# Performance work log

Measured on AMD Instinct MI355X. Metric: run time of the kernel, lower is better.

The kernel has to match this reference:

```python
import jax, jax.numpy as jnp
import numpy as np


def setup_inputs() -> dict:
    key = jax.random.key(0)
    k1, k2, k3, k4 = jax.random.split(key, 4)
    B, L, R, H, D = 64, 512, 512, 512, 256
    return {
        "lstm_lt": jax.random.normal(k1, (B, L, H), dtype=jnp.float32),
        "lstm_rt": jax.random.normal(k2, (B, R, H), dtype=jnp.float32),
        "atten_W": jax.random.normal(k3, (H, D), dtype=jnp.float32) * 0.05,
        "diagnoal_W": jax.random.normal(k4, (1, 1, D), dtype=jnp.float32) * 0.05,
    }


def reference(lstm_lt, lstm_rt, atten_W, diagnoal_W):
    # Projection (the original's broadcast-multiply-sum is exactly a GEMM):
    # atten_lt[b,l,d] = tanh(sum_h lstm_lt[b,l,h] * W[h,d]) * diag_W[d]
    atten_lt = jnp.tanh(jnp.einsum('blh,hd->bld', lstm_lt, atten_W)) * diagnoal_W
    atten_rt = jnp.tanh(jnp.einsum('brh,hd->brd', lstm_rt, atten_W))
    # batch_dot over the attention dim -> (B, L, R)
    atten_value = jnp.einsum('bld,brd->blr', atten_lt, atten_rt)
    # No masks supplied (len(inputs)==2 path); softmax over last axis.
    return jax.nn.softmax(atten_value, axis=-1)
```

## Files before the change

kernel.cpp:

```cpp
#include <hip/hip_runtime.h>

typedef __attribute__((ext_vector_type(8))) __bf16 bf16x8;
typedef __attribute__((ext_vector_type(4))) float f32x4;

#define DI __device__ __forceinline__

DI unsigned short f2bf(float x) {
  unsigned u = __float_as_uint(x);
  u += 0x7fffu + ((u >> 16) & 1u);
  return (unsigned short)(u >> 16);
}

DI float tanh_fast(float x) {
  float ax = fabsf(x);
  float e = __expf(-2.0f * ax);
  float t = (1.0f - e) / (1.0f + e);
  return x < 0.0f ? -t : t;
}

__global__ void k_wt(const float* __restrict__ W, unsigned short* __restrict__ Wt) {
  int n = blockIdx.x;
  int t = threadIdx.x;
  int k = t * 4;
  ushort4 v;
  v.x = f2bf(W[(k + 0) * 256 + n]);
  v.y = f2bf(W[(k + 1) * 256 + n]);
  v.z = f2bf(W[(k + 2) * 256 + n]);
  v.w = f2bf(W[(k + 3) * 256 + n]);
  *(ushort4*)&Wt[n * 512 + k] = v;
}

#define G1_LDA 72

__global__ __launch_bounds__(512) void k_proj(
    const float* __restrict__ Alt, const float* __restrict__ Art,
    const unsigned short* __restrict__ Wt, const float* __restrict__ diag,
    unsigned short* __restrict__ Olt, unsigned short* __restrict__ Ort) {
  __shared__ __align__(16) unsigned short As[128 * G1_LDA];
  __shared__ __align__(16) unsigned short Bs[256 * G1_LDA];

  int bx = blockIdx.x;
  bool is_lt = bx < 256;
  int m0 = (is_lt ? bx : bx - 256) * 128;
  const float* A = (is_lt ? Alt : Art) + (size_t)m0 * 512;
  unsigned short* O = (is_lt ? Olt : Ort) + (size_t)m0 * 256;

  int tid  = threadIdx.x;
  int lane = tid & 63;
  int wid  = tid >> 6;
  int wm   = wid >> 2;
  int wn   = wid & 3;
  int l15  = lane & 15;
  int quad = lane >> 4;

  f32x4 zero = {0.0f, 0.0f, 0.0f, 0.0f};
  f32x4 acc[4][4];
#pragma unroll
  for (int i = 0; i < 4; i++)
#pragma unroll
    for (int j = 0; j < 4; j++) acc[i][j] = zero;

  for (int k0 = 0; k0 < 512; k0 += 64) {
#pragma unroll
    for (int i = 0; i < 4; i++) {
      int seg = tid + i * 512;
      int r = seg >> 4;
      int c4 = seg & 15;
      f32x4 f = *(const f32x4*)&A[(size_t)r * 512 + k0 + c4 * 4];
      ushort4 v;
      v.x = f2bf(f.x); v.y = f2bf(f.y); v.z = f2bf(f.z); v.w = f2bf(f.w);
      *(ushort4*)&As[r * G1_LDA + c4 * 4] = v;
    }
#pragma unroll
    for (int i = 0; i < 4; i++) {
      int seg = tid + i * 512;
      int n = seg >> 3;
      int kc = seg & 7;
      *(uint4*)&Bs[n * G1_LDA + kc * 8] = *(const uint4*)&Wt[n * 512 + k0 + kc * 8];
    }
    __syncthreads();

#pragma unroll
    for (int ks = 0; ks < 2; ks++) {
      bf16x8 a[4], b[4];
#pragma unroll
      for (int mt = 0; mt < 4; mt++)
        a[mt] = *(const bf16x8*)&As[(wm * 64 + mt * 16 + l15) * G1_LDA + ks * 32 + quad * 8];
#pragma unroll
      for (int nt = 0; nt < 4; nt++)
        b[nt] = *(const bf16x8*)&Bs[(wn * 64 + nt * 16 + l15) * G1_LDA + ks * 32 + quad * 8];
#pragma unroll
      for (int mt = 0; mt < 4; mt++)
#pragma unroll
        for (int nt = 0; nt < 4; nt++)
          acc[mt][nt] = __builtin_amdgcn_mfma_f32_16x16x32_bf16(a[mt], b[nt], acc[mt][nt], 0, 0, 0);
    }
    __syncthreads();
  }

  float dscale[4];
#pragma unroll
  for (int nt = 0; nt < 4; nt++)
    dscale[nt] = is_lt ? diag[wn * 64 + nt * 16 + l15] : 1.0f;

#pragma unroll
  for (int mt = 0; mt < 4; mt++) {
#pragma unroll
    for (int r = 0; r < 4; r++) {
      int row = wm * 64 + mt * 16 + quad * 4 + r;
#pragma unroll
      for (int nt = 0; nt < 4; nt++) {
        int col = wn * 64 + nt * 16 + l15;
        float t = tanh_fast(acc[mt][nt][r]) * dscale[nt];
        O[(size_t)row * 256 + col] = f2bf(t);
      }
    }
  }
}

#define G2_LD 40

__global__ __launch_bounds__(512) void k_attn(
    const unsigned short* __restrict__ Lt, const unsigned short* __restrict__ Rt,
    float* __restrict__ Out) {
  __shared__ __align__(16) unsigned short Ls[64 * G2_LD];
  __shared__ __align__(16) unsigned short Rs[512 * G2_LD];
  __shared__ float red[8][64];
  __shared__ float rowv[64];

  int bx = blockIdx.x;
  int b  = bx >> 3;
  int l0 = (bx & 7) * 64;
  const unsigned short* Lb = Lt + ((size_t)b * 512 + l0) * 256;
  const unsigned short* Rb = Rt + (size_t)b * 512 * 256;
  float* Ob = Out + ((size_t)b * 512 + l0) * 512;

  int tid  = threadIdx.x;
  int lane = tid & 63;
  int wid  = tid >> 6;
  int l15  = lane & 15;
  int quad = lane >> 4;

  f32x4 zero = {0.0f, 0.0f, 0.0f, 0.0f};
  f32x4 acc[4][4];
#pragma unroll
  for (int i = 0; i < 4; i++)
#pragma unroll
    for (int j = 0; j < 4; j++) acc[i][j] = zero;

  for (int k0 = 0; k0 < 256; k0 += 32) {
    if (tid < 256) {
      int r = tid >> 2, kc = tid & 3;
      *(uint4*)&Ls[r * G2_LD + kc * 8] = *(const uint4*)&Lb[r * 256 + k0 + kc * 8];
    }
#pragma unroll
    for (int i = 0; i < 4; i++) {
      int seg = tid + i * 512;
      int r = seg >> 2, kc = seg & 3;
      *(uint4*)&Rs[r * G2_LD + kc * 8] = *(const uint4*)&Rb[r * 256 + k0 + kc * 8];
    }
    __syncthreads();

    bf16x8 a[4], bb[4];
#pragma unroll
    for (int mt = 0; mt < 4; mt++)
      a[mt] = *(const bf16x8*)&Ls[(mt * 16 + l15) * G2_LD + quad * 8];
#pragma unroll
    for (int nt = 0; nt < 4; nt++)
      bb[nt] = *(const bf16x8*)&Rs[(wid * 64 + nt * 16 + l15) * G2_LD + quad * 8];
#pragma unroll
    for (int mt = 0; mt < 4; mt++)
#pragma unroll
      for (int nt = 0; nt < 4; nt++)
        acc[mt][nt] = __builtin_amdgcn_mfma_f32_16x16x32_bf16(a[mt], bb[nt], acc[mt][nt], 0, 0, 0);
    __syncthreads();
  }

#pragma unroll
  for (int mt = 0; mt < 4; mt++) {
#pragma unroll
    for (int r = 0; r < 4; r++) {
      float m = fmaxf(fmaxf(acc[mt][0][r], acc[mt][1][r]),
                      fmaxf(acc[mt][2][r], acc[mt][3][r]));
      m = fmaxf(m, __shfl_xor(m, 1));
      m = fmaxf(m, __shfl_xor(m, 2));
      m = fmaxf(m, __shfl_xor(m, 4));
      m = fmaxf(m, __shfl_xor(m, 8));
      if (l15 == 0) red[wid][mt * 16 + quad * 4 + r] = m;
    }
  }
  __syncthreads();
  if (tid < 64) {
    float m = red[0][tid];
#pragma unroll
    for (int w = 1; w < 8; w++) m = fmaxf(m, red[w][tid]);
    rowv[tid] = m;
  }
  __syncthreads();

#pragma unroll
  for (int mt = 0; mt < 4; mt++) {
#pragma unroll
    for (int r = 0; r < 4; r++) {
      float base = rowv[mt * 16 + quad * 4 + r];
      float s = 0.0f;
#pragma unroll
      for (int nt = 0; nt < 4; nt++) {
        float e = __expf(acc[mt][nt][r] - base);
        acc[mt][nt][r] = e;
        s += e;
      }
      s += __shfl_xor(s, 1);
      s += __shfl_xor(s, 2);
      s += __shfl_xor(s, 4);
      s += __shfl_xor(s, 8);
      if (l15 == 0) red[wid][mt * 16 + quad * 4 + r] = s;
    }
  }
  __syncthreads();
  if (tid < 64) {
    float s = red[0][tid];
#pragma unroll
    for (int w = 1; w < 8; w++) s += red[w][tid];
    rowv[tid] = 1.0f / s;
  }
  __syncthreads();

#pragma unroll
  for (int mt = 0; mt < 4; mt++) {
#pragma unroll
    for (int r = 0; r < 4; r++) {
      int row = mt * 16 + quad * 4 + r;
      float inv = rowv[row];
#pragma unroll
      for (int nt = 0; nt < 4; nt++) {
        int col = wid * 64 + nt * 16 + l15;
        Ob[(size_t)row * 512 + col] = acc[mt][nt][r] * inv;
      }
    }
  }
}

extern "C" void kernel_launch(void* const* d_in, const int* in_sizes, int n_in,
                              void* d_out, int out_size, void* d_ws, size_t ws_size,
                              hipStream_t stream) {
  const float* lstm_lt = (const float*)d_in[0];
  const float* lstm_rt = (const float*)d_in[1];
  const float* W       = (const float*)d_in[2];
  const float* diag    = (const float*)d_in[3];
  float* out = (float*)d_out;

  unsigned short* Wt  = (unsigned short*)d_ws;
  unsigned short* Olt = (unsigned short*)((char*)d_ws + (size_t)256 * 512 * 2);
  unsigned short* Ort = Olt + (size_t)32768 * 256;

  k_wt<<<dim3(256), dim3(128), 0, stream>>>(W, Wt);
  k_proj<<<dim3(512), dim3(512), 0, stream>>>(lstm_lt, lstm_rt, Wt, diag, Olt, Ort);
  k_attn<<<dim3(512), dim3(512), 0, stream>>>(Olt, Ort, out);
}
```

Baseline: 238.5 us.

## Load MFMA fragments directly from global, drop LDS staging, remap blocks per XCD

Both GEMM kernels stop staging tiles through shared memory. Each wave now loads its bf16 (or fp32-converted) fragments straight from global memory into registers, which removes the per-k-step __syncthreads barriers. Blocks grow to 1024 threads with 32x64 tiles per wave, using launch_bounds(1024, 4). The attention kernel remaps block indices so that all row-blocks of one batch land on the same XCD, which should improve L2 reuse of the right-hand operand. The trade-off is redundant global/L2 reads and less coalesced fp32 loads for the projection input.

```diff
diff --git a/kernel.cpp b/kernel.cpp
--- a/kernel.cpp
+++ b/kernel.cpp
@@ -9,6 +9,13 @@
   unsigned u = __float_as_uint(x);
   u += 0x7fffu + ((u >> 16) & 1u);
   return (unsigned short)(u >> 16);
+}
+
+DI bf16x8 cvt8(f32x4 lo, f32x4 hi) {
+  bf16x8 r;
+  r[0] = (__bf16)lo.x; r[1] = (__bf16)lo.y; r[2] = (__bf16)lo.z; r[3] = (__bf16)lo.w;
+  r[4] = (__bf16)hi.x; r[5] = (__bf16)hi.y; r[6] = (__bf16)hi.z; r[7] = (__bf16)hi.w;
+  return r;
 }
 
 DI float tanh_fast(float x) {
@@ -30,15 +37,10 @@
   *(ushort4*)&Wt[n * 512 + k] = v;
 }
 
-#define G1_LDA 72
-
-__global__ __launch_bounds__(512) void k_proj(
+__global__ __launch_bounds__(1024, 4) void k_proj(
     const float* __restrict__ Alt, const float* __restrict__ Art,
     const unsigned short* __restrict__ Wt, const float* __restrict__ diag,
     unsigned short* __restrict__ Olt, unsigned short* __restrict__ Ort) {
-  __shared__ __align__(16) unsigned short As[128 * G1_LDA];
-  __shared__ __align__(16) unsigned short Bs[256 * G1_LDA];
-
   int bx = blockIdx.x;
   bool is_lt = bx < 256;
   int m0 = (is_lt ? bx : bx - 256) * 128;
@@ -48,89 +50,74 @@
   int tid  = threadIdx.x;
   int lane = tid & 63;
   int wid  = tid >> 6;
-  int wm   = wid >> 2;
-  int wn   = wid & 3;
+  int wmg  = wid >> 2;
+  int wng  = wid & 3;
   int l15  = lane & 15;
   int quad = lane >> 4;
 
+  const float* a0 = A + (size_t)(wmg * 32 + 0 * 16 + l15) * 512 + quad * 8;
+  const float* a1 = A + (size_t)(wmg * 32 + 1 * 16 + l15) * 512 + quad * 8;
+  const unsigned short* bp[4];
+#pragma unroll
+  for (int nt = 0; nt < 4; nt++)
+    bp[nt] = Wt + (size_t)(wng * 64 + nt * 16 + l15) * 512 + quad * 8;
+
   f32x4 zero = {0.0f, 0.0f, 0.0f, 0.0f};
-  f32x4 acc[4][4];
-#pragma unroll
-  for (int i = 0; i < 4; i++)
+  f32x4 acc[2][4];
+#pragma unroll
+  for (int i = 0; i < 2; i++)
 #pragma unroll
     for (int j = 0; j < 4; j++) acc[i][j] = zero;
 
-  for (int k0 = 0; k0 < 512; k0 += 64) {
-#pragma unroll
-    for (int i = 0; i < 4; i++) {
-      int seg = tid + i * 512;
-      int r = seg >> 4;
-      int c4 = seg & 15;
-      f32x4 f = *(const f32x4*)&A[(size_t)r * 512 + k0 + c4 * 4];
-      ushort4 v;
-      v.x = f2bf(f.x); v.y = f2bf(f.y); v.z = f2bf(f.z); v.w = f2bf(f.w);
-      *(ushort4*)&As[r * G1_LDA + c4 * 4] = v;
-    }
-#pragma unroll
-    for (int i = 0; i < 4; i++) {
-      int seg = tid + i * 512;
-      int n = seg >> 3;
-      int kc = seg & 7;
-      *(uint4*)&Bs[n * G1_LDA + kc * 8] = *(const uint4*)&Wt[n * 512 + k0 + kc * 8];
-    }
-    __syncthreads();
-
-#pragma unroll
-    for (int ks = 0; ks < 2; ks++) {
-      bf16x8 a[4], b[4];
-#pragma unroll
-      for (int mt = 0; mt < 4; mt++)
-        a[mt] = *(const bf16x8*)&As[(wm * 64 + mt * 16 + l15) * G1_LDA + ks * 32 + quad * 8];
+#pragma unroll 2
+  for (int k0 = 0; k0 < 512; k0 += 32) {
+    bf16x8 a[2], bb[4];
+    {
+      f32x4 lo0 = *(const f32x4*)(a0 + k0);
+      f32x4 hi0 = *(const f32x4*)(a0 + k0 + 4);
+      f32x4 lo1 = *(const f32x4*)(a1 + k0);
+      f32x4 hi1 = *(const f32x4*)(a1 + k0 + 4);
+      a[0] = cvt8(lo0, hi0);
+      a[1] = cvt8(lo1, hi1);
+    }
+#pragma unroll
+    for (int nt = 0; nt < 4; nt++)
+      bb[nt] = *(const bf16x8*)(bp[nt] + k0);
+#pragma unroll
+    for (int mt = 0; mt < 2; mt++)
 #pragma unroll
       for (int nt = 0; nt < 4; nt++)
-        b[nt] = *(const bf16x8*)&Bs[(wn * 64 + nt * 16 + l15) * G1_LDA + ks * 32 + quad * 8];
-#pragma unroll
-      for (int mt = 0; mt < 4; mt++)
-#pragma unroll
-        for (int nt = 0; nt < 4; nt++)
-          acc[mt][nt] = __builtin_amdgcn_mfma_f32_16x16x32_bf16(a[mt], b[nt], acc[mt][nt], 0, 0, 0);
-    }
-    __syncthreads();
+        acc[mt][nt] = __builtin_amdgcn_mfma_f32_16x16x32_bf16(a[mt], bb[nt], acc[mt][nt], 0, 0, 0);
   }
 
   float dscale[4];
 #pragma unroll
   for (int nt = 0; nt < 4; nt++)
-    dscale[nt] = is_lt ? diag[wn * 64 + nt * 16 + l15] : 1.0f;
-
-#pragma unroll
-  for (int mt = 0; mt < 4; mt++) {
-#pragma unroll
-    for (int r = 0; r < 4; r++) {
-      int row = wm * 64 + mt * 16 + quad * 4 + r;
+    dscale[nt] = is_lt ? diag[wng * 64 + nt * 16 + l15] : 1.0f;
+
+#pragma unroll
+  for (int mt = 0; mt < 2; mt++) {
+#pragma unroll
+    for (int r = 0; r < 4; r++) {
+      int row = wmg * 32 + mt * 16 + quad * 4 + r;
 #pragma unroll
       for (int nt = 0; nt < 4; nt++) {
-        int col = wn * 64 + nt * 16 + l15;
-        float t = tanh_fast(acc[mt][nt][r]) * dscale[nt];
-        O[(size_t)row * 256 + col] = f2bf(t);
+        int col = wng * 64 + nt * 16 + l15;
+        O[(size_t)row * 256 + col] = f2bf(tanh_fast(acc[mt][nt][r]) * dscale[nt]);
       }
     }
   }
 }
 
-#define G2_LD 40
-
-__global__ __launch_bounds__(512) void k_attn(
+__global__ __launch_bounds__(1024, 4) void k_attn(
     const unsigned short* __restrict__ Lt, const unsigned short* __restrict__ Rt,
     float* __restrict__ Out) {
-  __shared__ __align__(16) unsigned short Ls[64 * G2_LD];
-  __shared__ __align__(16) unsigned short Rs[512 * G2_LD];
   __shared__ float red[8][64];
   __shared__ float rowv[64];
 
   int bx = blockIdx.x;
-  int b  = bx >> 3;
-  int l0 = (bx & 7) * 64;
+  int b  = (bx & 7) * 8 + ((bx >> 3) & 7);
+  int l0 = (bx >> 6) * 64;
   const unsigned short* Lb = Lt + ((size_t)b * 512 + l0) * 256;
   const unsigned short* Rb = Rt + (size_t)b * 512 * 256;
   float* Ob = Out + ((size_t)b * 512 + l0) * 512;
@@ -138,46 +125,42 @@
   int tid  = threadIdx.x;
   int lane = tid & 63;
   int wid  = tid >> 6;
+  int wmg  = wid >> 3;
+  int wng  = wid & 7;
   int l15  = lane & 15;
   int quad = lane >> 4;
 
+  const unsigned short* ap0 = Lb + (size_t)(wmg * 32 + 0 * 16 + l15) * 256 + quad * 8;
+  const unsigned short* ap1 = Lb + (size_t)(wmg * 32 + 1 * 16 + l15) * 256 + quad * 8;
+  const unsigned short* bp[4];
+#pragma unroll
+  for (int nt = 0; nt < 4; nt++)
+    bp[nt] = Rb + (size_t)(wng * 64 + nt * 16 + l15) * 256 + quad * 8;
+
   f32x4 zero = {0.0f, 0.0f, 0.0f, 0.0f};
-  f32x4 acc[4][4];
-#pragma unroll
-  for (int i = 0; i < 4; i++)
+  f32x4 acc[2][4];
+#pragma unroll
+  for (int i = 0; i < 2; i++)
 #pragma unroll
     for (int j = 0; j < 4; j++) acc[i][j] = zero;
 
+#pragma unroll 2
   for (int k0 = 0; k0 < 256; k0 += 32) {
-    if (tid < 256) {
-      int r = tid >> 2, kc = tid & 3;
-      *(uint4*)&Ls[r * G2_LD + kc * 8] = *(const uint4*)&Lb[r * 256 + k0 + kc * 8];
-    }
-#pragma unroll
-    for (int i = 0; i < 4; i++) {
-      int seg = tid + i * 512;
-      int r = seg >> 2, kc = seg & 3;
-      *(uint4*)&Rs[r * G2_LD + kc * 8] = *(const uint4*)&Rb[r * 256 + k0 + kc * 8];
-    }
-    __syncthreads();
-
-    bf16x8 a[4], bb[4];
-#pragma unroll
-    for (int mt = 0; mt < 4; mt++)
-      a[mt] = *(const bf16x8*)&Ls[(mt * 16 + l15) * G2_LD + quad * 8];
+    bf16x8 a[2], bb[4];
+    a[0] = *(const bf16x8*)(ap0 + k0);
+    a[1] = *(const bf16x8*)(ap1 + k0);
 #pragma unroll
     for (int nt = 0; nt < 4; nt++)
-      bb[nt] = *(const bf16x8*)&Rs[(wid * 64 + nt * 16 + l15) * G2_LD + quad * 8];
-#pragma unroll
-    for (int mt = 0; mt < 4; mt++)
+      bb[nt] = *(const bf16x8*)(bp[nt] + k0);
+#pragma unroll
+    for (int mt = 0; mt < 2; mt++)
 #pragma unroll
       for (int nt = 0; nt < 4; nt++)
         acc[mt][nt] = __builtin_amdgcn_mfma_f32_16x16x32_bf16(a[mt], bb[nt], acc[mt][nt], 0, 0, 0);
-    __syncthreads();
-  }
-
-#pragma unroll
-  for (int mt = 0; mt < 4; mt++) {
+  }
+
+#pragma unroll
+  for (int mt = 0; mt < 2; mt++) {
 #pragma unroll
     for (int r = 0; r < 4; r++) {
       float m = fmaxf(fmaxf(acc[mt][0][r], acc[mt][1][r]),
@@ -186,7 +169,7 @@
       m = fmaxf(m, __shfl_xor(m, 2));
       m = fmaxf(m, __shfl_xor(m, 4));
       m = fmaxf(m, __shfl_xor(m, 8));
-      if (l15 == 0) red[wid][mt * 16 + quad * 4 + r] = m;
+      if (l15 == 0) red[wng][wmg * 32 + mt * 16 + quad * 4 + r] = m;
     }
   }
   __syncthreads();
@@ -199,10 +182,10 @@
   __syncthreads();
 
 #pragma unroll
-  for (int mt = 0; mt < 4; mt++) {
-#pragma unroll
-    for (int r = 0; r < 4; r++) {
-      float base = rowv[mt * 16 + quad * 4 + r];
+  for (int mt = 0; mt < 2; mt++) {
+#pragma unroll
+    for (int r = 0; r < 4; r++) {
+      float base = rowv[wmg * 32 + mt * 16 + quad * 4 + r];
       float s = 0.0f;
 #pragma unroll
       for (int nt = 0; nt < 4; nt++) {
@@ -214,7 +197,7 @@
       s += __shfl_xor(s, 2);
       s += __shfl_xor(s, 4);
       s += __shfl_xor(s, 8);
-      if (l15 == 0) red[wid][mt * 16 + quad * 4 + r] = s;
+      if (l15 == 0) red[wng][wmg * 32 + mt * 16 + quad * 4 + r] = s;
     }
   }
   __syncthreads();
@@ -227,14 +210,14 @@
   __syncthreads();
 
 #pragma unroll
-  for (int mt = 0; mt < 4; mt++) {
-#pragma unroll
-    for (int r = 0; r < 4; r++) {
-      int row = mt * 16 + quad * 4 + r;
+  for (int mt = 0; mt < 2; mt++) {
+#pragma unroll
+    for (int r = 0; r < 4; r++) {
+      int row = wmg * 32 + mt * 16 + quad * 4 + r;
       float inv = rowv[row];
 #pragma unroll
       for (int nt = 0; nt < 4; nt++) {
-        int col = wid * 64 + nt * 16 + l15;
+        int col = wng * 64 + nt * 16 + l15;
         Ob[(size_t)row * 512 + col] = acc[mt][nt][r] * inv;
       }
     }
@@ -255,6 +238,6 @@
   unsigned short* Ort = Olt + (size_t)32768 * 256;
 
   k_wt<<<dim3(256), dim3(128), 0, stream>>>(W, Wt);
-  k_proj<<<dim3(512), dim3(512), 0, stream>>>(lstm_lt, lstm_rt, Wt, diag, Olt, Ort);
-  k_attn<<<dim3(512), dim3(512), 0, stream>>>(Olt, Ort, out);
-}
+  k_proj<<<dim3(512), dim3(1024), 0, stream>>>(lstm_lt, lstm_rt, Wt, diag, Olt, Ort);
+  k_attn<<<dim3(512), dim3(1024), 0, stream>>>(Olt, Ort, out);
+}
```

After: 311.2 us. +30.5%, slower.

## Load GEMM tiles with direct global-to-LDS transfers and XOR-swizzled layouts

Applied to the files above, without the earlier changes.

Both the projection and attention kernels now fill shared memory with global_load_lds 16-byte direct transfers instead of going through registers. The layout uses XOR swizzles in place of padded strides. The projection kernel now keeps A tiles as fp32 in LDS and converts to bf16 when fragments are read, so register staging and conversion no longer sit on the load path. The attention kernel doubles its K step to 64 and remaps block indices so blocks sharing a batch are spread differently. Launch bounds now ask for higher occupancy, which adds register pressure, and the larger fp32 LDS tile may limit residency.

```diff
diff --git a/kernel.cpp b/kernel.cpp
--- a/kernel.cpp
+++ b/kernel.cpp
@@ -9,6 +9,13 @@
   unsigned u = __float_as_uint(x);
   u += 0x7fffu + ((u >> 16) & 1u);
   return (unsigned short)(u >> 16);
+}
+
+DI bf16x8 cvt8(f32x4 lo, f32x4 hi) {
+  bf16x8 r;
+  r[0] = (__bf16)lo.x; r[1] = (__bf16)lo.y; r[2] = (__bf16)lo.z; r[3] = (__bf16)lo.w;
+  r[4] = (__bf16)hi.x; r[5] = (__bf16)hi.y; r[6] = (__bf16)hi.z; r[7] = (__bf16)hi.w;
+  return r;
 }
 
 DI float tanh_fast(float x) {
@@ -16,6 +23,12 @@
   float e = __expf(-2.0f * ax);
   float t = (1.0f - e) / (1.0f + e);
   return x < 0.0f ? -t : t;
+}
+
+DI void glds16(const void* gptr, void* lptr) {
+  __builtin_amdgcn_global_load_lds(
+      (const __attribute__((address_space(1))) unsigned int*)gptr,
+      (__attribute__((address_space(3))) unsigned int*)lptr, 16, 0, 0);
 }
 
 __global__ void k_wt(const float* __restrict__ W, unsigned short* __restrict__ Wt) {
@@ -30,19 +43,17 @@
   *(ushort4*)&Wt[n * 512 + k] = v;
 }
 
-#define G1_LDA 72
-
-__global__ __launch_bounds__(512) void k_proj(
+__global__ __launch_bounds__(512, 4) void k_proj(
     const float* __restrict__ Alt, const float* __restrict__ Art,
     const unsigned short* __restrict__ Wt, const float* __restrict__ diag,
     unsigned short* __restrict__ Olt, unsigned short* __restrict__ Ort) {
-  __shared__ __align__(16) unsigned short As[128 * G1_LDA];
-  __shared__ __align__(16) unsigned short Bs[256 * G1_LDA];
+  __shared__ __align__(16) float As[128 * 64];
+  __shared__ __align__(16) unsigned short Bs[256 * 64];
 
   int bx = blockIdx.x;
   bool is_lt = bx < 256;
   int m0 = (is_lt ? bx : bx - 256) * 128;
-  const float* A = (is_lt ? Alt : Art) + (size_t)m0 * 512;
+  const char* Abase = (const char*)((is_lt ? Alt : Art) + (size_t)m0 * 512);
   unsigned short* O = (is_lt ? Olt : Ort) + (size_t)m0 * 256;
 
   int tid  = threadIdx.x;
@@ -52,6 +63,16 @@
   int wn   = wid & 3;
   int l15  = lane & 15;
   int quad = lane >> 4;
+  int r7   = l15 & 7;
+
+  int lr4 = lane >> 4, c16 = lane & 15;
+  int aoff = lr4 * 2048 + ((c16 ^ lr4) << 4);
+  int lr8 = lane >> 3, s8 = lane & 7;
+  int boff = lr8 * 1024 + ((s8 ^ lr8) << 4);
+
+  const char* Bbase = (const char*)Wt;
+  char* AsB = (char*)As;
+  char* BsB = (char*)Bs;
 
   f32x4 zero = {0.0f, 0.0f, 0.0f, 0.0f};
   f32x4 acc[4][4];
@@ -63,20 +84,14 @@
   for (int k0 = 0; k0 < 512; k0 += 64) {
 #pragma unroll
     for (int i = 0; i < 4; i++) {
-      int seg = tid + i * 512;
-      int r = seg >> 4;
-      int c4 = seg & 15;
-      f32x4 f = *(const f32x4*)&A[(size_t)r * 512 + k0 + c4 * 4];
-      ushort4 v;
-      v.x = f2bf(f.x); v.y = f2bf(f.y); v.z = f2bf(f.z); v.w = f2bf(f.w);
-      *(ushort4*)&As[r * G1_LDA + c4 * 4] = v;
+      int j = wid * 4 + i;
+      glds16(Abase + (size_t)j * 8192 + (size_t)k0 * 4 + (aoff ^ ((j & 1) << 6)),
+             AsB + j * 1024);
     }
 #pragma unroll
     for (int i = 0; i < 4; i++) {
-      int seg = tid + i * 512;
-      int n = seg >> 3;
-      int kc = seg & 7;
-      *(uint4*)&Bs[n * G1_LDA + kc * 8] = *(const uint4*)&Wt[n * 512 + k0 + kc * 8];
+      int j = wid * 4 + i;
+      glds16(Bbase + (size_t)j * 8192 + (size_t)k0 * 2 + boff, BsB + j * 1024);
     }
     __syncthreads();
 
@@ -84,11 +99,19 @@
     for (int ks = 0; ks < 2; ks++) {
       bf16x8 a[4], b[4];
 #pragma unroll
-      for (int mt = 0; mt < 4; mt++)
-        a[mt] = *(const bf16x8*)&As[(wm * 64 + mt * 16 + l15) * G1_LDA + ks * 32 + quad * 8];
-#pragma unroll
-      for (int nt = 0; nt < 4; nt++)
-        b[nt] = *(const bf16x8*)&Bs[(wn * 64 + nt * 16 + l15) * G1_LDA + ks * 32 + quad * 8];
+      for (int mt = 0; mt < 4; mt++) {
+        int row = wm * 64 + mt * 16 + l15;
+        int c0 = ks * 8 + quad * 2;
+        f32x4 lo = *(const f32x4*)(AsB + row * 256 + (((c0    ) ^ r7) << 4));
+        f32x4 hi = *(const f32x4*)(AsB + row * 256 + (((c0 + 1) ^ r7) << 4));
+        a[mt] = cvt8(lo, hi);
+      }
+#pragma unroll
+      for (int nt = 0; nt < 4; nt++) {
+        int row = wn * 64 + nt * 16 + l15;
+        int c = ks * 4 + quad;
+        b[nt] = *(const bf16x8*)(BsB + row * 128 + ((c ^ r7) << 4));
+      }
 #pragma unroll
       for (int mt = 0; mt < 4; mt++)
 #pragma unroll
@@ -111,28 +134,25 @@
 #pragma unroll
       for (int nt = 0; nt < 4; nt++) {
         int col = wn * 64 + nt * 16 + l15;
-        float t = tanh_fast(acc[mt][nt][r]) * dscale[nt];
-        O[(size_t)row * 256 + col] = f2bf(t);
-      }
-    }
-  }
-}
-
-#define G2_LD 40
-
-__global__ __launch_bounds__(512) void k_attn(
+        O[(size_t)row * 256 + col] = f2bf(tanh_fast(acc[mt][nt][r]) * dscale[nt]);
+      }
+    }
+  }
+}
+
+__global__ __launch_bounds__(512, 4) void k_attn(
     const unsigned short* __restrict__ Lt, const unsigned short* __restrict__ Rt,
     float* __restrict__ Out) {
-  __shared__ __align__(16) unsigned short Ls[64 * G2_LD];
-  __shared__ __align__(16) unsigned short Rs[512 * G2_LD];
+  __shared__ __align__(16) unsigned short Ls[64 * 64];
+  __shared__ __align__(16) unsigned short Rs[512 * 64];
   __shared__ float red[8][64];
   __shared__ float rowv[64];
 
   int bx = blockIdx.x;
-  int b  = bx >> 3;
-  int l0 = (bx & 7) * 64;
-  const unsigned short* Lb = Lt + ((size_t)b * 512 + l0) * 256;
-  const unsigned short* Rb = Rt + (size_t)b * 512 * 256;
+  int b  = (bx & 7) * 8 + ((bx >> 3) & 7);
+  int l0 = (bx >> 6) * 64;
+  const char* Lb = (const char*)(Lt + ((size_t)b * 512 + l0) * 256);
+  const char* Rb = (const char*)(Rt + (size_t)b * 512 * 256);
   float* Ob = Out + ((size_t)b * 512 + l0) * 512;
 
   int tid  = threadIdx.x;
@@ -140,6 +160,13 @@
   int wid  = tid >> 6;
   int l15  = lane & 15;
   int quad = lane >> 4;
+  int r7   = l15 & 7;
+
+  int lr8 = lane >> 3, s8 = lane & 7;
+  int goff = lr8 * 512 + ((s8 ^ lr8) << 4);
+
+  char* LsB = (char*)Ls;
+  char* RsB = (char*)Rs;
 
   f32x4 zero = {0.0f, 0.0f, 0.0f, 0.0f};
   f32x4 acc[4][4];
@@ -148,31 +175,36 @@
 #pragma unroll
     for (int j = 0; j < 4; j++) acc[i][j] = zero;
 
-  for (int k0 = 0; k0 < 256; k0 += 32) {
-    if (tid < 256) {
-      int r = tid >> 2, kc = tid & 3;
-      *(uint4*)&Ls[r * G2_LD + kc * 8] = *(const uint4*)&Lb[r * 256 + k0 + kc * 8];
-    }
-#pragma unroll
-    for (int i = 0; i < 4; i++) {
-      int seg = tid + i * 512;
-      int r = seg >> 2, kc = seg & 3;
-      *(uint4*)&Rs[r * G2_LD + kc * 8] = *(const uint4*)&Rb[r * 256 + k0 + kc * 8];
-    }
-    __syncthreads();
-
-    bf16x8 a[4], bb[4];
-#pragma unroll
-    for (int mt = 0; mt < 4; mt++)
-      a[mt] = *(const bf16x8*)&Ls[(mt * 16 + l15) * G2_LD + quad * 8];
-#pragma unroll
-    for (int nt = 0; nt < 4; nt++)
-      bb[nt] = *(const bf16x8*)&Rs[(wid * 64 + nt * 16 + l15) * G2_LD + quad * 8];
-#pragma unroll
-    for (int mt = 0; mt < 4; mt++)
-#pragma unroll
-      for (int nt = 0; nt < 4; nt++)
-        acc[mt][nt] = __builtin_amdgcn_mfma_f32_16x16x32_bf16(a[mt], bb[nt], acc[mt][nt], 0, 0, 0);
+  for (int k0 = 0; k0 < 256; k0 += 64) {
+    glds16(Lb + (size_t)wid * 4096 + (size_t)k0 * 2 + goff, LsB + wid * 1024);
+#pragma unroll
+    for (int i = 0; i < 8; i++) {
+      int j = wid * 8 + i;
+      glds16(Rb + (size_t)j * 4096 + (size_t)k0 * 2 + goff, RsB + j * 1024);
+    }
+    __syncthreads();
+
+#pragma unroll
+    for (int ks = 0; ks < 2; ks++) {
+      bf16x8 a[4], bb[4];
+#pragma unroll
+      for (int mt = 0; mt < 4; mt++) {
+        int row = mt * 16 + l15;
+        int c = ks * 4 + quad;
+        a[mt] = *(const bf16x8*)(LsB + row * 128 + ((c ^ r7) << 4));
+      }
+#pragma unroll
+      for (int nt = 0; nt < 4; nt++) {
+        int row = wid * 64 + nt * 16 + l15;
+        int c = ks * 4 + quad;
+        bb[nt] = *(const bf16x8*)(RsB + row * 128 + ((c ^ r7) << 4));
+      }
+#pragma unroll
+      for (int mt = 0; mt < 4; mt++)
+#pragma unroll
+        for (int nt = 0; nt < 4; nt++)
+          acc[mt][nt] = __builtin_amdgcn_mfma_f32_16x16x32_bf16(a[mt], bb[nt], acc[mt][nt], 0, 0, 0);
+    }
     __syncthreads();
   }
 
```

New measurement: 208.0 us. 12.8% less time.
